# Optimization experiments

Measured on AMD Instinct MI355X. Metric: run time of the kernel, lower is better.

## Reference

```python
import jax, jax.numpy as jnp
import numpy as np
import math

B, S, D, H = 2, 2048, 1024, 16
DH = D // H  # dim_per_head = 64


def setup_inputs() -> dict:
    key = jax.random.key(0)
    ks = jax.random.split(key, 12)
    s = 1.0 / math.sqrt(D)
    return {
        "key": jax.random.normal(ks[0], (B, S, D), jnp.float32),
        "value": jax.random.normal(ks[1], (B, S, D), jnp.float32),
        "query": jax.random.normal(ks[2], (B, S, D), jnp.float32),
        "mask": jax.random.randint(ks[3], (B, S, S), 0, 2).astype(bool),
        "Wq": jax.random.normal(ks[4], (D, D), jnp.float32) * s,
        "bq": jnp.zeros((D,), jnp.float32),
        "Wk": jax.random.normal(ks[5], (D, D), jnp.float32) * s,
        "bk": jnp.zeros((D,), jnp.float32),
        "Wv": jax.random.normal(ks[6], (D, D), jnp.float32) * s,
        "bv": jnp.zeros((D,), jnp.float32),
        "Wo": jax.random.normal(ks[7], (D, D), jnp.float32) * s,
        "bo": jnp.zeros((D,), jnp.float32),
    }


def _shape(x):
    # [B, S, D] -> [B, H, S, DH]
    return x.reshape(B, -1, H, DH).transpose(0, 2, 1, 3)


def reference(key, value, query, mask, Wq, bq, Wk, bk, Wv, bv, Wo, bo):
    q = _shape(query @ Wq.T + bq)  # [B,H,Sq,DH]
    k = _shape(key @ Wk.T + bk)    # [B,H,Sk,DH]
    v = _shape(value @ Wv.T + bv)  # [B,H,Sk,DH]
    q = q / jnp.sqrt(jnp.asarray(DH, q.dtype))
    scores = jnp.einsum("bhqd,bhkd->bhqk", q, k)
    scores = jnp.where(mask[:, None, :, :], jnp.asarray(-1e18, scores.dtype), scores)
    attn = jax.nn.softmax(scores, axis=-1)
    # dropout is identity in eval/deterministic reference
    ctx = jnp.einsum("bhqk,bhkd->bhqd", attn, v)
    ctx = ctx.transpose(0, 2, 1, 3).reshape(B, -1, D)  # unshape
    return ctx @ Wo.T + bo
```

## Files before the change

### kernel.cpp

```cpp
#include <hip/hip_runtime.h>
#include <math.h>


constexpr int Bc  = 2;
constexpr int Sc  = 2048;
constexpr int Dc  = 1024;
constexpr int Hc  = 16;
constexpr int DHc = 64;
constexpr int BSc = Bc * Sc;

constexpr float LOG2E = 1.4426950408889634f;

typedef __bf16 bf16x8 __attribute__((ext_vector_type(8)));
typedef __bf16 bf16x4 __attribute__((ext_vector_type(4)));
typedef __bf16 bf16x2 __attribute__((ext_vector_type(2)));
typedef float  f32x4  __attribute__((ext_vector_type(4)));
typedef float  f32x16 __attribute__((ext_vector_type(16)));
typedef unsigned uint32x2 __attribute__((ext_vector_type(2)));
typedef unsigned uint32x4 __attribute__((ext_vector_type(4)));

#define GLDS16(gp, lp) __builtin_amdgcn_global_load_lds( \
    (const __attribute__((address_space(1))) void*)(gp), \
    (__attribute__((address_space(3))) void*)(lp), 16, 0, 0)

__global__ __launch_bounds__(256)
void prep(const float* __restrict__ W0, const float* __restrict__ W1,
          const float* __restrict__ W2, const float* __restrict__ W3,
          __bf16* __restrict__ Whi,
          const float* __restrict__ A0, const float* __restrict__ A1,
          const float* __restrict__ A2, __bf16* __restrict__ Abf,
          const int* __restrict__ mask, unsigned long long* __restrict__ mpk)
{
    const int bid = blockIdx.x;
    const int tid = threadIdx.x;

    if (bid < 4096) {
        const float* src[4] = {W0, W1, W2, W3};
        const int z  = bid >> 10;
        const int bx = bid & 1023;
        const size_t idx = ((size_t)bx * 256 + tid) * 4;
        const float4 v = *(const float4*)&src[z][idx];
        bf16x4 o;
        o[0] = (__bf16)v.x; o[1] = (__bf16)v.y;
        o[2] = (__bf16)v.z; o[3] = (__bf16)v.w;
        *(bf16x4*)&Whi[(size_t)z * Dc * Dc + idx] = o;
    } else if (bid < 10240) {
        const float* src[3] = {A0, A1, A2};
        const int lin = bid - 4096;
        const int z  = lin >> 11;
        const int bx = lin & 2047;
        const size_t idx = ((size_t)bx * 256 + tid) * 8;
        const float4 a = *(const float4*)&src[z][idx];
        const float4 b = *(const float4*)&src[z][idx + 4];
        bf16x8 o;
        o[0] = (__bf16)a.x; o[1] = (__bf16)a.y; o[2] = (__bf16)a.z; o[3] = (__bf16)a.w;
        o[4] = (__bf16)b.x; o[5] = (__bf16)b.y; o[6] = (__bf16)b.z; o[7] = (__bf16)b.w;
        *(bf16x8*)&Abf[(size_t)z * BSc * Dc + idx] = o;
    } else {
        const int bx   = bid - 10240;
        const int lane = tid & 63;
        const size_t waveBase = ((size_t)bx * 4 + (tid >> 6)) * 256;
        unsigned long long b0 = __ballot(mask[waveBase + lane]        != 0);
        unsigned long long b1 = __ballot(mask[waveBase + 64 + lane]   != 0);
        unsigned long long b2 = __ballot(mask[waveBase + 128 + lane]  != 0);
        unsigned long long b3 = __ballot(mask[waveBase + 192 + lane]  != 0);
        if (lane == 0) {
            unsigned long long* dst = mpk + (waveBase >> 6);
            dst[0] = b0; dst[1] = b1; dst[2] = b2; dst[3] = b3;
        }
    }
}

template<int KD>
__device__ __forceinline__ void sweep128bb(const __bf16* __restrict__ A,
                                           const __bf16* __restrict__ Wh,
                                           char* AsB, char* WsB,
                                           int gm0, int gn0, f32x4 acc[4][4])
{
    const int tid  = threadIdx.x;
    const int w    = tid >> 6;
    const int lane = tid & 63;
    const int cc   = lane & 15;
    const int g    = lane >> 4;
    const int wm   = (w & 1) * 64;
    const int wn   = (w >> 1) * 64;

    int wrow[4], wchk[4];
#pragma unroll
    for (int r = 0; r < 4; ++r) {
        const int L = r * 256 + tid;
        wrow[r] = L >> 3;
        wchk[r] = (L & 7) ^ (wrow[r] & 7);
    }

#pragma unroll
    for (int r = 0; r < 4; ++r) {
        GLDS16(Wh + (size_t)(gn0 + wrow[r]) * KD + wchk[r] * 8,
               WsB + (r * 256 + tid) * 16);
        GLDS16(A + (size_t)(gm0 + wrow[r]) * KD + wchk[r] * 8,
               AsB + (r * 256 + tid) * 16);
    }

    for (int it = 0; it < KD / 64; ++it) {
        const char* As = AsB + (it & 1) * 16384;
        const char* Ws = WsB + (it & 1) * 16384;
        __syncthreads();

        if (it + 1 < KD / 64) {
            const int kn = (it + 1) * 64;
            char* Wn = WsB + ((it + 1) & 1) * 16384;
            char* An = AsB + ((it + 1) & 1) * 16384;
#pragma unroll
            for (int r = 0; r < 4; ++r) {
                GLDS16(Wh + (size_t)(gn0 + wrow[r]) * KD + kn + wchk[r] * 8,
                       Wn + (r * 256 + tid) * 16);
                GLDS16(A + (size_t)(gm0 + wrow[r]) * KD + kn + wchk[r] * 8,
                       An + (r * 256 + tid) * 16);
            }
        }

        __builtin_amdgcn_s_setprio(1);
#pragma unroll
        for (int kk = 0; kk < 2; ++kk) {
            const int cb4 = (kk * 4 + g) << 4;
            bf16x8 af[4], bfr[4];
#pragma unroll
            for (int mt = 0; mt < 4; ++mt) {
                const int row = wm + mt * 16 + cc;
                af[mt] = *(const bf16x8*)(As + row * 128 + (cb4 ^ ((row & 7) << 4)));
            }
#pragma unroll
            for (int nt = 0; nt < 4; ++nt) {
                const int row = wn + nt * 16 + cc;
                bfr[nt] = *(const bf16x8*)(Ws + row * 128 + (cb4 ^ ((row & 7) << 4)));
            }
#pragma unroll
            for (int mt = 0; mt < 4; ++mt)
#pragma unroll
                for (int nt = 0; nt < 4; ++nt)
                    acc[mt][nt] = __builtin_amdgcn_mfma_f32_16x16x32_bf16(
                        af[mt], bfr[nt], acc[mt][nt], 0, 0, 0);
        }
        __builtin_amdgcn_s_setprio(0);
    }
}

__device__ __forceinline__ void sweep64p(const __bf16* __restrict__ Ahi,
                                         const __bf16* __restrict__ Alo,
                                         const __bf16* __restrict__ Wh,
                                         char* WsB, char* AhB, char* AlB,
                                         int gm0, int gn0, f32x4 acc[2][4])
{
    const int tid  = threadIdx.x;
    const int w    = tid >> 6;
    const int lane = tid & 63;
    const int cc   = lane & 15;
    const int g    = lane >> 4;
    const int wm   = (w & 1) * 32;
    const int wn   = (w >> 1) * 64;

    int wrow[4], wchk[4];
#pragma unroll
    for (int r = 0; r < 4; ++r) {
        const int L = r * 256 + tid;
        wrow[r] = L >> 3;
        wchk[r] = (L & 7) ^ (wrow[r] & 7);
    }
    int arow[2], achk[2];
#pragma unroll
    for (int r = 0; r < 2; ++r) {
        const int L = r * 256 + tid;
        arow[r] = L >> 3;
        achk[r] = (L & 7) ^ (arow[r] & 7);
    }

#pragma unroll
    for (int r = 0; r < 4; ++r)
        GLDS16(Wh + (size_t)(gn0 + wrow[r]) * Dc + wchk[r] * 8,
               WsB + (r * 256 + tid) * 16);
#pragma unroll
    for (int r = 0; r < 2; ++r) {
        GLDS16(Ahi + (size_t)(gm0 + arow[r]) * Dc + achk[r] * 8,
               AhB + (r * 256 + tid) * 16);
        GLDS16(Alo + (size_t)(gm0 + arow[r]) * Dc + achk[r] * 8,
               AlB + (r * 256 + tid) * 16);
    }

    for (int it = 0; it < Dc / 64; ++it) {
        const char* Ws = WsB + (it & 1) * 16384;
        const char* Ah = AhB + (it & 1) * 8192;
        const char* Al = AlB + (it & 1) * 8192;
        __syncthreads();

        if (it + 1 < Dc / 64) {
            const int kn = (it + 1) * 64;
            char* Wn = WsB + ((it + 1) & 1) * 16384;
            char* Hn = AhB + ((it + 1) & 1) * 8192;
            char* Ln = AlB + ((it + 1) & 1) * 8192;
#pragma unroll
            for (int r = 0; r < 4; ++r)
                GLDS16(Wh + (size_t)(gn0 + wrow[r]) * Dc + kn + wchk[r] * 8,
                       Wn + (r * 256 + tid) * 16);
#pragma unroll
            for (int r = 0; r < 2; ++r) {
                GLDS16(Ahi + (size_t)(gm0 + arow[r]) * Dc + kn + achk[r] * 8,
                       Hn + (r * 256 + tid) * 16);
                GLDS16(Alo + (size_t)(gm0 + arow[r]) * Dc + kn + achk[r] * 8,
                       Ln + (r * 256 + tid) * 16);
            }
        }

        __builtin_amdgcn_s_setprio(1);
#pragma unroll
        for (int kk = 0; kk < 2; ++kk) {
            const int cb4 = (kk * 4 + g) << 4;
            bf16x8 ahi[2], alo[2], bfr[4];
#pragma unroll
            for (int mt = 0; mt < 2; ++mt) {
                const int row = wm + mt * 16 + cc;
                const int off = row * 128 + (cb4 ^ ((row & 7) << 4));
                ahi[mt] = *(const bf16x8*)(Ah + off);
                alo[mt] = *(const bf16x8*)(Al + off);
            }
#pragma unroll
            for (int nt = 0; nt < 4; ++nt) {
                const int row = wn + nt * 16 + cc;
                bfr[nt] = *(const bf16x8*)(Ws + row * 128 + (cb4 ^ ((row & 7) << 4)));
            }
#pragma unroll
            for (int mt = 0; mt < 2; ++mt)
#pragma unroll
                for (int nt = 0; nt < 4; ++nt) {
                    acc[mt][nt] = __builtin_amdgcn_mfma_f32_16x16x32_bf16(
                        ahi[mt], bfr[nt], acc[mt][nt], 0, 0, 0);
                    acc[mt][nt] = __builtin_amdgcn_mfma_f32_16x16x32_bf16(
                        alo[mt], bfr[nt], acc[mt][nt], 0, 0, 0);
                }
        }
        __builtin_amdgcn_s_setprio(0);
    }
}

__global__ __launch_bounds__(256)
void qkv_mfma(const __bf16* __restrict__ Abf, const __bf16* __restrict__ Whi,
              const float* __restrict__ bq, const float* __restrict__ bk,
              const float* __restrict__ bv,
              __bf16* __restrict__ Qo, __bf16* __restrict__ Ko, __bf16* __restrict__ Vt)
{
    __shared__ __align__(16) char smem[65536];

    const int z = blockIdx.y;
    const float* bias = (z == 0) ? bq : (z == 1) ? bk : bv;
    const float scale = (z == 0) ? 0.125f * LOG2E : 1.0f;
    const __bf16* A   = Abf + (size_t)z * BSc * Dc;
    const __bf16* Wh  = Whi + (size_t)z * Dc * Dc;

    const int lb  = (blockIdx.x & 7) * 32 + (blockIdx.x >> 3);
    const int idx = lb & 31;
    const int gm0 = ((lb >> 5) * 4 + (idx & 3)) * 128;
    const int gn0 = (idx >> 2) * 128;

    f32x4 acc[4][4];
#pragma unroll
    for (int mt = 0; mt < 4; ++mt)
#pragma unroll
        for (int nt = 0; nt < 4; ++nt) acc[mt][nt] = {0.f, 0.f, 0.f, 0.f};

    sweep128bb<Dc>(A, Wh, smem, smem + 32768, gm0, gn0, acc);

    const int tid = threadIdx.x;
    const int w = tid >> 6, lane = tid & 63;
    const int cc = lane & 15, g = lane >> 4;
    const int wm = (w & 1) * 64, wn = (w >> 1) * 64;

    float bias4[4];
#pragma unroll
    for (int nt = 0; nt < 4; ++nt) bias4[nt] = bias[gn0 + wn + nt * 16 + cc];

    if (z == 2) {
#pragma unroll
        for (int mt = 0; mt < 4; ++mt)
#pragma unroll
            for (int nt = 0; nt < 4; ++nt) {
                const int col = gn0 + wn + nt * 16 + cc;
                const int h = col >> 6, dh = col & 63;
                const int row0 = gm0 + wm + mt * 16 + g * 4;
                const int b = row0 >> 11, s0 = row0 & 2047;
                bf16x4 vv;
#pragma unroll
                for (int reg = 0; reg < 4; ++reg)
                    vv[reg] = (__bf16)(acc[mt][nt][reg] + bias4[nt]);
                *(bf16x4*)&Vt[(((size_t)(b * Hc + h)) * DHc + dh) * Sc + s0] = vv;
            }
    } else {
        __bf16* O = (z == 0) ? Qo : Ko;
#pragma unroll
        for (int mt = 0; mt < 4; ++mt)
#pragma unroll
            for (int nt = 0; nt < 4; ++nt) {
                const int col = gn0 + wn + nt * 16 + cc;
                const int h = col >> 6, dh = col & 63;
#pragma unroll
                for (int reg = 0; reg < 4; ++reg) {
                    const int row = gm0 + wm + mt * 16 + g * 4 + reg;
                    const int b = row >> 11, s = row & 2047;
                    O[(((size_t)(b * Hc + h)) * Sc + s) * DHc + dh] =
                        (__bf16)((acc[mt][nt][reg] + bias4[nt]) * scale);
                }
            }
    }
}

__global__ __launch_bounds__(256)
void out_mfma(const __bf16* __restrict__ ctxHi, const __bf16* __restrict__ ctxLo,
              const __bf16* __restrict__ Wohi,
              const float* __restrict__ bo, float* __restrict__ out)
{
    __shared__ __align__(16) char smem[65536];

    const int lb = (blockIdx.x & 7) * 64 + (blockIdx.x >> 3);
    const int gm0 = ((lb >> 6) * 8 + (lb & 7)) * 64;
    const int gn0 = ((lb >> 3) & 7) * 128;

    f32x4 acc[2][4];
#pragma unroll
    for (int mt = 0; mt < 2; ++mt)
#pragma unroll
        for (int nt = 0; nt < 4; ++nt) acc[mt][nt] = {0.f, 0.f, 0.f, 0.f};

    sweep64p(ctxHi, ctxLo, Wohi, smem, smem + 32768, smem + 49152, gm0, gn0, acc);

    const int tid = threadIdx.x;
    const int w = tid >> 6, lane = tid & 63;
    const int cc = lane & 15, g = lane >> 4;
    const int wm = (w & 1) * 32, wn = (w >> 1) * 64;

    float bias4[4];
#pragma unroll
    for (int nt = 0; nt < 4; ++nt) bias4[nt] = bo[gn0 + wn + nt * 16 + cc];

#pragma unroll
    for (int mt = 0; mt < 2; ++mt)
#pragma unroll
        for (int nt = 0; nt < 4; ++nt) {
            const int col = gn0 + wn + nt * 16 + cc;
#pragma unroll
            for (int reg = 0; reg < 4; ++reg) {
                const int row = gm0 + wm + mt * 16 + g * 4 + reg;
                out[(size_t)row * Dc + col] = acc[mt][nt][reg] + bias4[nt];
            }
        }
}

__device__ __forceinline__ void stage_pair(const __bf16* Kb, const __bf16* Vtb,
                                           char* H, int t0,
                                           int rowi0, int ski0, int ci0,
                                           int rowi1, int ski1, int ci1)
{
#pragma unroll
    for (int s = 0; s < 2; ++s) {
        char* B = H + s * 16384;
        const int kn = (t0 + s) * 64;
        GLDS16(Kb + (size_t)(kn + rowi0) * DHc + ski0 * 8, B + ci0 * 16);
        GLDS16(Vtb + (size_t)rowi0 * Sc + kn + ski0 * 8, B + 8192 + ci0 * 16);
        GLDS16(Kb + (size_t)(kn + rowi1) * DHc + ski1 * 8, B + ci1 * 16);
        GLDS16(Vtb + (size_t)rowi1 * Sc + kn + ski1 * 8, B + 8192 + ci1 * 16);
    }
}

__device__ __forceinline__ void tile_step(const char* Ks, const char* Vs,
                                          const bf16x8 qa[4], const f32x16& zb,
                                          unsigned long long mw, int c, int u,
                                          float lp[4], f32x16 o[2])
{
    f32x16 sc[2];
    __builtin_amdgcn_s_setprio(1);
#pragma unroll
    for (int nt = 0; nt < 2; ++nt) {
        const int row = nt * 32 + c;
        const int rx  = (((row & 7) ^ ((row >> 3) & 7)) << 4);
        const bf16x8 kb0 = *(const bf16x8*)(Ks + row * 128 + ((u * 16) ^ rx));
        f32x16 z = __builtin_amdgcn_mfma_f32_32x32x16_bf16(kb0, qa[0], zb, 0, 0, 0);
#pragma unroll
        for (int ch = 1; ch < 4; ++ch) {
            const bf16x8 kb = *(const bf16x8*)
                (Ks + row * 128 + ((ch * 32 + u * 16) ^ rx));
            z = __builtin_amdgcn_mfma_f32_32x32x16_bf16(kb, qa[ch], z, 0, 0, 0);
        }
        sc[nt] = z;
    }
    __builtin_amdgcn_s_setprio(0);

    unsigned pk[2][4][2];
#pragma unroll
    for (int nt = 0; nt < 2; ++nt)
#pragma unroll
        for (int rr = 0; rr < 4; ++rr) {
            const unsigned nib =
                (unsigned)(mw >> (nt * 32 + rr * 8 + u * 4)) & 0xFu;
            float pv[4];
#pragma unroll
            for (int r = 0; r < 4; ++r) {
                float p = __builtin_amdgcn_exp2f(sc[nt][rr * 4 + r]);
                p = (nib & (1u << r)) ? 0.f : p;
                lp[rr] += p;
                pv[r] = p;
            }
            bf16x2 t0; t0[0] = (__bf16)pv[0]; t0[1] = (__bf16)pv[1];
            bf16x2 t1; t1[0] = (__bf16)pv[2]; t1[1] = (__bf16)pv[3];
            pk[nt][rr][0] = __builtin_bit_cast(unsigned, t0);
            pk[nt][rr][1] = __builtin_bit_cast(unsigned, t1);
        }

    bf16x8 pa[4];
#pragma unroll
    for (int kc = 0; kc < 4; ++kc) {
        const int nt = kc >> 1;
        const int r0 = (kc & 1) * 2;
        uint32x2 w0 = __builtin_amdgcn_permlane32_swap(
            pk[nt][r0][0], pk[nt][r0 + 1][0], false, false);
        uint32x2 w1 = __builtin_amdgcn_permlane32_swap(
            pk[nt][r0][1], pk[nt][r0 + 1][1], false, false);
        uint32x4 wds;
        wds[0] = w0[0]; wds[1] = w1[0]; wds[2] = w0[1]; wds[3] = w1[1];
        pa[kc] = __builtin_bit_cast(bf16x8, wds);
    }

    __builtin_amdgcn_s_setprio(1);
#pragma unroll
    for (int dt = 0; dt < 2; ++dt) {
        const int row = dt * 32 + c;
        const int rx  = (((row & 7) ^ ((row >> 3) & 7)) << 4);
#pragma unroll
        for (int kc = 0; kc < 4; ++kc) {
            const bf16x8 vb = *(const bf16x8*)
                (Vs + row * 128 + ((kc * 32 + u * 16) ^ rx));
            o[dt] = __builtin_amdgcn_mfma_f32_32x32x16_bf16(pa[kc], vb, o[dt], 0, 0, 0);
        }
    }
    __builtin_amdgcn_s_setprio(0);
}

__global__ __launch_bounds__(256, 2)
void attn_mfma(const __bf16* __restrict__ Q, const __bf16* __restrict__ K,
               const __bf16* __restrict__ Vt,
               const unsigned long long* __restrict__ mp,
               __bf16* __restrict__ ctxHi, __bf16* __restrict__ ctxLo)
{
    __shared__ __align__(16) char smem[65536];

    const int tid  = threadIdx.x;
    const int w    = tid >> 6;
    const int lane = tid & 63;
    const int c    = lane & 31;
    const int u    = lane >> 5;

    const int bx  = blockIdx.x;
    const int lb  = (bx & 7) * 64 + (bx >> 3);
    const int bh  = lb >> 4;
    const int qb  = lb & 15;
    const int b   = bh >> 4;
    const int h   = bh & 15;
    const int qw  = qb * 128 + w * 32;

    const __bf16* Qb  = Q  + (size_t)bh * Sc * DHc;
    const __bf16* Kb  = K  + (size_t)bh * Sc * DHc;
    const __bf16* Vtb = Vt + (size_t)bh * DHc * Sc;

    bf16x8 qa[4];
#pragma unroll
    for (int ch = 0; ch < 4; ++ch)
        qa[ch] = *(const bf16x8*)&Qb[(size_t)(qw + c) * DHc + ch * 16 + u * 8];

    f32x16 o[2], zb;
#pragma unroll
    for (int i = 0; i < 16; ++i) { o[0][i] = 0.f; o[1][i] = 0.f; zb[i] = -24.f; }
    float lp[4] = {0.f, 0.f, 0.f, 0.f};

    const int ci0 = tid,        ci1 = 256 + tid;
    const int rowi0 = ci0 >> 3, rowi1 = ci1 >> 3;
    const int ski0 = (ci0 & 7) ^ (rowi0 & 7) ^ ((rowi0 >> 3) & 7);
    const int ski1 = (ci1 & 7) ^ (rowi1 & 7) ^ ((rowi1 >> 3) & 7);

    const size_t mbase = ((size_t)(b * Sc + qw + c) << 5);

    stage_pair(Kb, Vtb, smem, 0, rowi0, ski0, ci0, rowi1, ski1, ci1);

    for (int j = 0; j < 16; ++j) {
        __syncthreads();
        if (j + 1 < 16)
            stage_pair(Kb, Vtb, smem + ((j + 1) & 1) * 32768, 2 * j + 2,
                       rowi0, ski0, ci0, rowi1, ski1, ci1);

        const char* H = smem + (j & 1) * 32768;
        const unsigned long long mw0 = mp[mbase + 2 * j];
        const unsigned long long mw1 = mp[mbase + 2 * j + 1];

        tile_step(H,         H + 8192,  qa, zb, mw0, c, u, lp, o);
        tile_step(H + 16384, H + 24576, qa, zb, mw1, c, u, lp, o);
    }

    float lsum = (lp[0] + lp[1]) + (lp[2] + lp[3]);
    lsum += __shfl_xor(lsum, 32);
    const float linv = 1.0f / lsum;

    float inv[16];
#pragma unroll
    for (int i = 0; i < 16; ++i)
        inv[i] = __shfl(linv, (i & 3) + 8 * (i >> 2) + 4 * u);

#pragma unroll
    for (int dt = 0; dt < 2; ++dt)
#pragma unroll
        for (int i = 0; i < 16; ++i) {
            const int q = qw + (i & 3) + 8 * (i >> 2) + 4 * u;
            const size_t idx = ((size_t)b * Sc + q) * Dc + h * 64 + dt * 32 + c;
            const float v = o[dt][i] * inv[i];
            const __bf16 hi = (__bf16)v;
            ctxHi[idx] = hi;
            ctxLo[idx] = (__bf16)(v - (float)hi);
        }
}

extern "C" void kernel_launch(void* const* d_in, const int* in_sizes, int n_in,
                              void* d_out, int out_size, void* d_ws, size_t ws_size,
                              hipStream_t stream)
{
    const float* key   = (const float*)d_in[0];
    const float* value = (const float*)d_in[1];
    const float* query = (const float*)d_in[2];
    const int*   mask  = (const int*)  d_in[3];
    const float* Wq    = (const float*)d_in[4];
    const float* bq    = (const float*)d_in[5];
    const float* Wk    = (const float*)d_in[6];
    const float* bk    = (const float*)d_in[7];
    const float* Wv    = (const float*)d_in[8];
    const float* bv    = (const float*)d_in[9];
    const float* Wo    = (const float*)d_in[10];
    const float* bo    = (const float*)d_in[11];
    float* out = (float*)d_out;

    char* wsb = (char*)d_ws;
    __bf16* Qbf  = (__bf16*)(wsb);
    __bf16* Kbf  = (__bf16*)(wsb + ((size_t)8  << 20));
    __bf16* Vt   = (__bf16*)(wsb + ((size_t)16 << 20));
    unsigned long long* mpk = (unsigned long long*)(wsb + ((size_t)32 << 20));
    __bf16* Whi  = (__bf16*)(wsb + ((size_t)33 << 20));
    __bf16* ctxHi = (__bf16*)(wsb + ((size_t)41 << 20));
    __bf16* ctxLo = (__bf16*)(wsb + ((size_t)49 << 20));
    __bf16* Abf  = (__bf16*)(wsb + ((size_t)57 << 20));

    prep<<<dim3(18432), 256, 0, stream>>>(Wq, Wk, Wv, Wo, Whi,
                                          query, key, value, Abf,
                                          mask, mpk);

    dim3 gqkv(256, 3);
    qkv_mfma<<<gqkv, 256, 0, stream>>>(Abf, Whi, bq, bk, bv, Qbf, Kbf, Vt);

    attn_mfma<<<dim3(512), 256, 0, stream>>>(Qbf, Kbf, Vt, mpk, ctxHi, ctxLo);

    out_mfma<<<dim3(512), 256, 0, stream>>>(ctxHi, ctxLo, Whi + (size_t)3 * Dc * Dc,
                                            bo, out);
}
```

Baseline: 246.9 us.

## Interleave softmax of second K tile with PV MFMAs of first tile

Restructures the per-iteration attention loop so both QK^T tiles are computed up front, then the exp/mask/pack work for the second tile is interleaved chunk-by-chunk with the PV MFMAs of the first tile. The aim is to overlap VALU exp2 work with matrix-core work inside a single wave instead of running them serially. It raises register pressure, since two score tiles are live at once, which under launch_bounds(256,2) risks spills or lower overlap if the compiler reorders the instructions.

After: 251.5 us. About the same (+1.9%).

```diff
diff --git a/kernel.cpp b/kernel.cpp
--- a/kernel.cpp
+++ b/kernel.cpp
@@ -368,13 +368,10 @@
     }
 }
 
-__device__ __forceinline__ void tile_step(const char* Ks, const char* Vs,
-                                          const bf16x8 qa[4], const f32x16& zb,
-                                          unsigned long long mw, int c, int u,
-                                          float lp[4], f32x16 o[2])
-{
-    f32x16 sc[2];
-    __builtin_amdgcn_s_setprio(1);
+__device__ __forceinline__ void qk_tile(const char* Ks, const bf16x8 qa[4],
+                                        const f32x16& zb, int c, int u,
+                                        f32x16& s0, f32x16& s1)
+{
 #pragma unroll
     for (int nt = 0; nt < 2; ++nt) {
         const int row = nt * 32 + c;
@@ -387,58 +384,45 @@
                 (Ks + row * 128 + ((ch * 32 + u * 16) ^ rx));
             z = __builtin_amdgcn_mfma_f32_32x32x16_bf16(kb, qa[ch], z, 0, 0, 0);
         }
-        sc[nt] = z;
-    }
-    __builtin_amdgcn_s_setprio(0);
-
-    unsigned pk[2][4][2];
-#pragma unroll
-    for (int nt = 0; nt < 2; ++nt)
-#pragma unroll
-        for (int rr = 0; rr < 4; ++rr) {
-            const unsigned nib =
-                (unsigned)(mw >> (nt * 32 + rr * 8 + u * 4)) & 0xFu;
-            float pv[4];
-#pragma unroll
-            for (int r = 0; r < 4; ++r) {
-                float p = __builtin_amdgcn_exp2f(sc[nt][rr * 4 + r]);
-                p = (nib & (1u << r)) ? 0.f : p;
-                lp[rr] += p;
-                pv[r] = p;
-            }
-            bf16x2 t0; t0[0] = (__bf16)pv[0]; t0[1] = (__bf16)pv[1];
-            bf16x2 t1; t1[0] = (__bf16)pv[2]; t1[1] = (__bf16)pv[3];
-            pk[nt][rr][0] = __builtin_bit_cast(unsigned, t0);
-            pk[nt][rr][1] = __builtin_bit_cast(unsigned, t1);
-        }
-
-    bf16x8 pa[4];
+        if (nt == 0) s0 = z; else s1 = z;
+    }
+}
+
+__device__ __forceinline__ void sm_chunk(int chunk,
+                                         const f32x16& s0, const f32x16& s1,
+                                         unsigned long long mw, int u,
+                                         float lp[4], unsigned pk[8][2])
+{
+    const int nt = chunk >> 2, rr = chunk & 3;
+    const unsigned nib = (unsigned)(mw >> (nt * 32 + rr * 8 + u * 4)) & 0xFu;
+    float pv[4];
+#pragma unroll
+    for (int r = 0; r < 4; ++r) {
+        float p = __builtin_amdgcn_exp2f((nt == 0) ? s0[rr * 4 + r]
+                                                   : s1[rr * 4 + r]);
+        p = (nib & (1u << r)) ? 0.f : p;
+        lp[rr] += p;
+        pv[r] = p;
+    }
+    bf16x2 t0; t0[0] = (__bf16)pv[0]; t0[1] = (__bf16)pv[1];
+    bf16x2 t1; t1[0] = (__bf16)pv[2]; t1[1] = (__bf16)pv[3];
+    pk[chunk][0] = __builtin_bit_cast(unsigned, t0);
+    pk[chunk][1] = __builtin_bit_cast(unsigned, t1);
+}
+
+__device__ __forceinline__ void redist(const unsigned pk[8][2], bf16x8 pa[4])
+{
 #pragma unroll
     for (int kc = 0; kc < 4; ++kc) {
-        const int nt = kc >> 1;
-        const int r0 = (kc & 1) * 2;
+        const int c0 = (kc >> 1) * 4 + (kc & 1) * 2;
         uint32x2 w0 = __builtin_amdgcn_permlane32_swap(
-            pk[nt][r0][0], pk[nt][r0 + 1][0], false, false);
+            pk[c0][0], pk[c0 + 1][0], false, false);
         uint32x2 w1 = __builtin_amdgcn_permlane32_swap(
-            pk[nt][r0][1], pk[nt][r0 + 1][1], false, false);
+            pk[c0][1], pk[c0 + 1][1], false, false);
         uint32x4 wds;
         wds[0] = w0[0]; wds[1] = w1[0]; wds[2] = w0[1]; wds[3] = w1[1];
         pa[kc] = __builtin_bit_cast(bf16x8, wds);
     }
-
-    __builtin_amdgcn_s_setprio(1);
-#pragma unroll
-    for (int dt = 0; dt < 2; ++dt) {
-        const int row = dt * 32 + c;
-        const int rx  = (((row & 7) ^ ((row >> 3) & 7)) << 4);
-#pragma unroll
-        for (int kc = 0; kc < 4; ++kc) {
-            const bf16x8 vb = *(const bf16x8*)
-                (Vs + row * 128 + ((kc * 32 + u * 16) ^ rx));
-            o[dt] = __builtin_amdgcn_mfma_f32_32x32x16_bf16(pa[kc], vb, o[dt], 0, 0, 0);
-        }
-    }
-    __builtin_amdgcn_s_setprio(0);
 }
 
 __global__ __launch_bounds__(256, 2)
@@ -496,8 +480,53 @@
         const unsigned long long mw0 = mp[mbase + 2 * j];
         const unsigned long long mw1 = mp[mbase + 2 * j + 1];
 
-        tile_step(H,         H + 8192,  qa, zb, mw0, c, u, lp, o);
-        tile_step(H + 16384, H + 24576, qa, zb, mw1, c, u, lp, o);
+        f32x16 a0, a1, b0, b1;
+        __builtin_amdgcn_s_setprio(1);
+        qk_tile(H,         qa, zb, c, u, a0, a1);
+        qk_tile(H + 16384, qa, zb, c, u, b0, b1);
+        __builtin_amdgcn_s_setprio(0);
+
+        unsigned pk0[8][2];
+#pragma unroll
+        for (int chk = 0; chk < 8; ++chk)
+            sm_chunk(chk, a0, a1, mw0, u, lp, pk0);
+        bf16x8 pa0[4];
+        redist(pk0, pa0);
+
+        unsigned pk1[8][2];
+        const char* Vs0 = H + 8192;
+        __builtin_amdgcn_s_setprio(1);
+#pragma unroll
+        for (int dt = 0; dt < 2; ++dt) {
+            const int row = dt * 32 + c;
+            const int rx  = (((row & 7) ^ ((row >> 3) & 7)) << 4);
+#pragma unroll
+            for (int kc = 0; kc < 4; ++kc) {
+                const bf16x8 vb = *(const bf16x8*)
+                    (Vs0 + row * 128 + ((kc * 32 + u * 16) ^ rx));
+                o[dt] = __builtin_amdgcn_mfma_f32_32x32x16_bf16(pa0[kc], vb, o[dt], 0, 0, 0);
+                sm_chunk(dt * 4 + kc, b0, b1, mw1, u, lp, pk1);
+            }
+        }
+        __builtin_amdgcn_s_setprio(0);
+
+        bf16x8 pa1[4];
+        redist(pk1, pa1);
+
+        const char* Vs1 = H + 24576;
+        __builtin_amdgcn_s_setprio(1);
+#pragma unroll
+        for (int dt = 0; dt < 2; ++dt) {
+            const int row = dt * 32 + c;
+            const int rx  = (((row & 7) ^ ((row >> 3) & 7)) << 4);
+#pragma unroll
+            for (int kc = 0; kc < 4; ++kc) {
+                const bf16x8 vb = *(const bf16x8*)
+                    (Vs1 + row * 128 + ((kc * 32 + u * 16) ^ rx));
+                o[dt] = __builtin_amdgcn_mfma_f32_32x32x16_bf16(pa1[kc], vb, o[dt], 0, 0, 0);
+            }
+        }
+        __builtin_amdgcn_s_setprio(0);
     }
 
     float lsum = (lp[0] + lp[1]) + (lp[2] + lp[3]);
```
